# Kernel tuning notes

Measured on AMD Instinct MI355X. Metric: run time of the kernel, lower is better.

## Reference

```python
import jax, jax.numpy as jnp
import numpy as np

EPS = 1e-5

def _bn(x, g, b, m, v):
    # inference-mode BatchNorm2d over channel dim of NCHW
    inv = jax.lax.rsqrt(v + EPS)
    return (x - m[None, :, None, None]) * (g * inv)[None, :, None, None] + b[None, :, None, None]

def _conv1x1(x, w, b):
    # x: [B,C,H,W], w: [O,C], b: [O]
    return jnp.einsum('bchw,oc->bohw', x, w) + b[None, :, None, None]

def setup_inputs() -> dict:
    key = jax.random.key(0)
    ks = jax.random.split(key, 20)
    B, C, H, W = 16, 512, 64, 64
    C2, C4 = C // 2, C // 4
    d = {}
    d['x'] = jax.random.normal(ks[0], (B, C, H, W), jnp.float32)
    # query_conv_p1: Conv2d(512->256, k1) + BN + ReLU
    d['q1_w'] = jax.random.normal(ks[1], (C2, C), jnp.float32) * (1.0 / np.sqrt(C))
    d['q1_b'] = jax.random.normal(ks[2], (C2,), jnp.float32) * 0.01
    d['bn1_g'] = jax.random.uniform(ks[3], (C2,), jnp.float32, 0.5, 1.5)
    d['bn1_b'] = jax.random.normal(ks[4], (C2,), jnp.float32) * 0.01
    d['bn1_m'] = jax.random.normal(ks[5], (C2,), jnp.float32) * 0.01
    d['bn1_v'] = jax.random.uniform(ks[6], (C2,), jnp.float32, 0.5, 1.5)
    # query_conv_p2: Conv2d(256->128, k1) + BN + ReLU
    d['q2_w'] = jax.random.normal(ks[7], (C4, C2), jnp.float32) * (1.0 / np.sqrt(C2))
    d['q2_b'] = jax.random.normal(ks[8], (C4,), jnp.float32) * 0.01
    d['bn2_g'] = jax.random.uniform(ks[9], (C4,), jnp.float32, 0.5, 1.5)
    d['bn2_b'] = jax.random.normal(ks[10], (C4,), jnp.float32) * 0.01
    d['bn2_m'] = jax.random.normal(ks[11], (C4,), jnp.float32) * 0.01
    d['bn2_v'] = jax.random.uniform(ks[12], (C4,), jnp.float32, 0.5, 1.5)
    # py1_prop: Conv1d(256->256, k1)  (py2_prop is never used in forward)
    d['p1_w'] = jax.random.normal(ks[13], (C2, C2), jnp.float32) * (1.0 / np.sqrt(C2))
    d['p1_b'] = jax.random.normal(ks[14], (C2,), jnp.float32) * 0.01
    # fusion_conv: Conv2d(512->512, k3, pad 1) + BN + ReLU
    d['fus_w'] = jax.random.normal(ks[15], (C, C, 3, 3), jnp.float32) * (1.0 / np.sqrt(C * 9))
    d['fus_b'] = jax.random.normal(ks[16], (C,), jnp.float32) * 0.01
    d['bn3_g'] = jax.random.uniform(ks[17], (C,), jnp.float32, 0.5, 1.5)
    d['bn3_b'] = jax.random.normal(ks[18], (C,), jnp.float32) * 0.01
    d['bn3_m'] = jnp.zeros((C,), jnp.float32)
    d['bn3_v'] = jnp.ones((C,), jnp.float32)
    # gamma: torch init is zeros(1); use small random so the attention branch is live
    d['gamma'] = jax.random.normal(ks[19], (1,), jnp.float32) * 0.1
    return d

def reference(x, q1_w, q1_b, bn1_g, bn1_b, bn1_m, bn1_v,
              q2_w, q2_b, bn2_g, bn2_b, bn2_m, bn2_v,
              p1_w, p1_b, fus_w, fus_b, bn3_g, bn3_b, bn3_m, bn3_v, gamma):
    B, C, H, W = x.shape
    C2, C4 = C // 2, C // 4
    py1 = jax.nn.relu(_bn(_conv1x1(x, q1_w, q1_b), bn1_g, bn1_b, bn1_m, bn1_v))   # [B,256,H,W]
    py2 = jax.nn.relu(_bn(_conv1x1(py1, q2_w, q2_b), bn2_g, bn2_b, bn2_m, bn2_v))  # [B,128,H,W]
    pq1 = py1.reshape(B, C2, -1)   # [B,256,HW]
    pk1 = x.reshape(B, C, -1)      # [B,512,HW]
    # energy_py1 = pq1 @ pk1^T -> [B,256,512]; Conv1d(k1) over channel dim; permute -> [B,512,256]
    e1 = jnp.einsum('bcn,bdn->bcd', pq1, pk1)
    e1 = jnp.einsum('oc,bcd->bod', p1_w, e1) + p1_b[None, :, None]
    e1 = e1.transpose(0, 2, 1)     # [B,512,256]
    pq2 = py2.reshape(B, C4, -1)   # [B,128,HW]
    # energy_py2 = (pq2 @ py1^T).permute -> [B,256,128]; same py1_prop conv applied
    e2 = jnp.einsum('bcn,bdn->bcd', pq2, py1.reshape(B, C2, -1)).transpose(0, 2, 1)  # [B,256,128]
    e2 = jnp.einsum('oc,bcd->bod', p1_w, e2) + p1_b[None, :, None]                    # [B,256,128]
    energy = jnp.einsum('bce,bed->bcd', e1, e2)  # [B,512,128]
    energy_new = jnp.max(energy, axis=-1, keepdims=True) - energy
    attention = jax.nn.softmax(energy_new, axis=-1)  # [B,512,128]
    out = jnp.einsum('bcd,bdn->bcn', attention, pq2)  # [B,512,HW]
    out = out.reshape(B, C, H, W)
    out = gamma[0] * out + x
    out = jax.lax.conv_general_dilated(out, fus_w, window_strides=(1, 1),
                                       padding=((1, 1), (1, 1)),
                                       dimension_numbers=('NCHW', 'OIHW', 'NCHW'))
    out = out + fus_b[None, :, None, None]
    out = jax.nn.relu(_bn(out, bn3_g, bn3_b, bn3_m, bn3_v))
    return out
```

## Files before the change

### kernel.cpp

```cpp
#include <hip/hip_runtime.h>
#include <math.h>

#define BATCH 16
#define CH    512
#define CH2   256
#define CH4   128
#define HH    64
#define WW    64
#define HWSZ  4096
#define EPSV  1e-5f
#define HP 66
#define WP 66

typedef _Float16 f16x8 __attribute__((ext_vector_type(8)));
typedef float    f32x4 __attribute__((ext_vector_type(4)));

#define GLOBAL_AS __attribute__((address_space(1)))
#define LDS_AS    __attribute__((address_space(3)))

__device__ __forceinline__ void gload16(const void* g, void* l) {
    __builtin_amdgcn_global_load_lds((const GLOBAL_AS unsigned int*)g,
                                     (LDS_AS unsigned int*)l, 16, 0, 0);
}

__device__ __forceinline__ ushort f2h(float v) {
    _Float16 h = (_Float16)v;
    return *(ushort*)&h;
}
__device__ __forceinline__ float h2f(ushort u) {
    _Float16 h = *(_Float16*)&u;
    return (float)h;
}

__global__ void prep_params(
    const float* __restrict__ q1_b, const float* __restrict__ g1, const float* __restrict__ b1,
    const float* __restrict__ m1, const float* __restrict__ v1,
    const float* __restrict__ q2_b, const float* __restrict__ g2, const float* __restrict__ b2,
    const float* __restrict__ m2, const float* __restrict__ v2,
    const float* __restrict__ fus_b, const float* __restrict__ g3, const float* __restrict__ b3,
    const float* __restrict__ m3, const float* __restrict__ v3,
    float* __restrict__ s1, float* __restrict__ t1,
    float* __restrict__ s2, float* __restrict__ t2,
    float* __restrict__ s3, float* __restrict__ t3)
{
    int i = threadIdx.x;
    if (i < CH2) { float s = g1[i] * rsqrtf(v1[i] + EPSV); s1[i] = s; t1[i] = (q1_b[i] - m1[i]) * s + b1[i]; }
    if (i < CH4) { float s = g2[i] * rsqrtf(v2[i] + EPSV); s2[i] = s; t2[i] = (q2_b[i] - m2[i]) * s + b2[i]; }
    if (i < CH)  { float s = g3[i] * rsqrtf(v3[i] + EPSV); s3[i] = s; t3[i] = (fus_b[i] - m3[i]) * s + b3[i]; }
}

__global__ void transpose_p1(const float* __restrict__ p1w, float* __restrict__ p1T)
{
    int c = blockIdx.x;
    int o = threadIdx.x;
    p1T[c * CH2 + o] = p1w[o * CH2 + c];
}

__global__ void repack_w(const float* __restrict__ fw, ushort* __restrict__ wH)
{
    int o = blockIdx.x;
    int c = threadIdx.x;
    const float* src = fw + ((size_t)o * CH + c) * 9;
    #pragma unroll
    for (int t = 0; t < 9; ++t)
        wH[((size_t)t * CH + o) * CH + c] = f2h(src[t]);
}

__global__ void cvt_h(const float* __restrict__ s, ushort* __restrict__ d, int n)
{
    int i = blockIdx.x * blockDim.x + threadIdx.x;
    if (i < n) d[i] = f2h(s[i]);
}

__global__ void zero_buf(uint4* __restrict__ p, int n)
{
    const uint4 z = make_uint4(0u, 0u, 0u, 0u);
    for (int i = blockIdx.x * blockDim.x + threadIdx.x; i < n; i += gridDim.x * blockDim.x)
        p[i] = z;
}

__global__ __launch_bounds__(256)
void cvt_x(const float* __restrict__ x, ushort* __restrict__ xHc, ushort* __restrict__ xHp)
{
    __shared__ float t[64][68];
    const int b  = blockIdx.z;
    const int c0 = blockIdx.y * 64;
    const int p0 = blockIdx.x * 64;
    const int tid = threadIdx.x;
    const int tx = tid & 15, ty = tid >> 4;

    const float* xb = x + ((size_t)b * CH + c0) * HWSZ + p0;
    #pragma unroll
    for (int it = 0; it < 4; ++it) {
        const int r = ty + it * 16;
        float4 v = *(const float4*)&xb[(size_t)r * HWSZ + tx * 4];
        *(float4*)&t[r][tx * 4] = v;
        ushort4 u = make_ushort4(f2h(v.x), f2h(v.y), f2h(v.z), f2h(v.w));
        *(ushort4*)&xHc[((size_t)b * CH + c0 + r) * HWSZ + p0 + tx * 4] = u;
    }
    __syncthreads();
    #pragma unroll
    for (int it = 0; it < 4; ++it) {
        const int p = ty + it * 16;
        const int c = tx * 4;
        ushort4 u = make_ushort4(f2h(t[c + 0][p]), f2h(t[c + 1][p]),
                                 f2h(t[c + 2][p]), f2h(t[c + 3][p]));
        *(ushort4*)&xHp[((size_t)b * HWSZ + p0 + p) * CH + c0 + c] = u;
    }
}

template<int EPI>
__global__ __launch_bounds__(256)
void hgemm(const ushort* __restrict__ A, const ushort* __restrict__ B,
           void* __restrict__ C0, void* __restrict__ C1,
           int N, int KP, int ldA, int ldB, int ldHp,
           long sA, long sB, long sC0, long sC1, long pStride,
           const float* __restrict__ scale, const float* __restrict__ shift,
           const ushort* __restrict__ XHp, const float* __restrict__ gamma)
{
    __shared__ alignas(16) ushort As[4096];
    __shared__ alignas(16) ushort Bs[4096];

    const int b  = blockIdx.z & 15;
    const int pk = blockIdx.z >> 4;
    const int m0 = blockIdx.y * 128;
    const int n0 = blockIdx.x * 128;
    const int kBase = pk * KP;

    const int tid  = threadIdx.x;
    const int lane = tid & 63;
    const int wv   = tid >> 6;
    const int wm   = wv >> 1;
    const int wn   = wv & 1;

    const int cpart = (lane & 3) * 8;
    const int prow  = lane >> 2;
    const int rA0 = wv * 32 + prow;
    const int rA1 = rA0 + 16;

    const ushort* Ag = A + (size_t)b * sA;
    const ushort* Bg = B + (size_t)b * sB;
    const ushort* aSrc0 = Ag + (size_t)(m0 + rA0) * ldA + cpart + kBase;
    const ushort* aSrc1 = Ag + (size_t)(m0 + rA1) * ldA + cpart + kBase;
    const ushort* bSrc0 = Bg + (size_t)(n0 + rA0) * ldB + cpart + kBase;
    const ushort* bSrc1 = Bg + (size_t)(n0 + rA1) * ldB + cpart + kBase;
    ushort* AsW = &As[wv * 1024];
    ushort* BsW = &Bs[wv * 1024];

    const int fr = lane & 15, fg = lane >> 4;
    const int aOff = (wm * 64 + fr) * 32 + fg * 8;
    const int bOff = (wn * 64 + fr) * 32 + fg * 8;

    f32x4 acc[4][4];
    const f32x4 vzero = {0.f, 0.f, 0.f, 0.f};
    #pragma unroll
    for (int i = 0; i < 4; ++i)
        #pragma unroll
        for (int j = 0; j < 4; ++j) acc[i][j] = vzero;

    for (int k0 = 0; k0 < KP; k0 += 32) {
        gload16(aSrc0 + k0, AsW);
        gload16(aSrc1 + k0, AsW + 512);
        gload16(bSrc0 + k0, BsW);
        gload16(bSrc1 + k0, BsW + 512);
        __syncthreads();

        f16x8 aF[4], bF[4];
        #pragma unroll
        for (int mi = 0; mi < 4; ++mi) aF[mi] = *(const f16x8*)&As[aOff + mi * 512];
        #pragma unroll
        for (int ni = 0; ni < 4; ++ni) bF[ni] = *(const f16x8*)&Bs[bOff + ni * 512];
        #pragma unroll
        for (int mi = 0; mi < 4; ++mi)
            #pragma unroll
            for (int ni = 0; ni < 4; ++ni)
                acc[mi][ni] = __builtin_amdgcn_mfma_f32_16x16x32_f16(aF[mi], bF[ni], acc[mi][ni], 0, 0, 0);
        __syncthreads();
    }

    #pragma unroll
    for (int mi = 0; mi < 4; ++mi) {
        const int mBase = m0 + wm * 64 + mi * 16 + fg * 4;
        #pragma unroll
        for (int ni = 0; ni < 4; ++ni) {
            const int n = n0 + wn * 64 + ni * 16 + fr;
            if constexpr (EPI == 0) {
                ushort us[4];
                #pragma unroll
                for (int reg = 0; reg < 4; ++reg) {
                    const int m = mBase + reg;
                    float v = fmaxf(acc[mi][ni][reg] * scale[m] + shift[m], 0.0f);
                    us[reg] = f2h(v);
                    ((ushort*)C0)[(size_t)b * sC0 + (size_t)m * N + n] = us[reg];
                }
                *(ushort4*)&((ushort*)C1)[(size_t)b * sC1 + (size_t)n * ldHp + mBase] =
                    make_ushort4(us[0], us[1], us[2], us[3]);
            }
            if constexpr (EPI == 1) {
                float* C = (float*)C0 + pk * pStride + (size_t)b * sC0;
                #pragma unroll
                for (int reg = 0; reg < 4; ++reg)
                    C[(size_t)(mBase + reg) * N + n] = acc[mi][ni][reg];
            }
            if constexpr (EPI == 2) {
                const int h = n >> 6, w = n & 63;
                const float g = gamma[0];
                ushort4 xv = *(const ushort4*)&XHp[((size_t)b * HWSZ + n) * CH + mBase];
                ushort4 pk4;
                pk4.x = f2h(g * acc[mi][ni][0] + h2f(xv.x));
                pk4.y = f2h(g * acc[mi][ni][1] + h2f(xv.y));
                pk4.z = f2h(g * acc[mi][ni][2] + h2f(xv.z));
                pk4.w = f2h(g * acc[mi][ni][3] + h2f(xv.w));
                *(ushort4*)&((ushort*)C0)[((size_t)(b * HP + h + 1) * WP + (w + 1)) * CH + mBase] = pk4;
            }
        }
    }
}

__global__ void reduce_parts(float* __restrict__ dst, const float* __restrict__ src,
                             int n4, int parts, long pstride)
{
    for (int i = blockIdx.x * blockDim.x + threadIdx.x; i < n4; i += gridDim.x * blockDim.x) {
        float4 s = ((const float4*)src)[i];
        for (int p = 1; p < parts; ++p) {
            const float4 v = *(const float4*)&src[(size_t)p * pstride + (size_t)i * 4];
            s.x += v.x; s.y += v.y; s.z += v.z; s.w += v.w;
        }
        ((float4*)dst)[i] = s;
    }
}

template<int EPI>
__global__ __launch_bounds__(256)
void gemm_ab(const float* __restrict__ A, const float* __restrict__ Bm,
             float* __restrict__ Cm,
             int M, int N, int K,
             long sA, long sB, long sC,
             const float* __restrict__ shift)
{
    __shared__ float As[16][68];
    __shared__ float Bs[16][68];

    const int b   = blockIdx.z;
    const float* Ab = A  + (long)b * sA;
    const float* Bb = Bm + (long)b * sB;

    const int m0 = blockIdx.y * 64;
    const int n0 = blockIdx.x * 64;
    const int tid = threadIdx.x;
    const int tx = tid & 15;
    const int ty = tid >> 4;

    const int a_m = tid >> 2;
    const int a_k = (tid & 3) * 4;
    const int b_k = tid >> 4;
    const int b_n = (tid & 15) * 4;

    float acc[4][4] = {};

    for (int k0 = 0; k0 < K; k0 += 16) {
        float4 av = *(const float4*)&Ab[(long)(m0 + a_m) * K + k0 + a_k];
        float4 bv = *(const float4*)&Bb[(long)(k0 + b_k) * N + n0 + b_n];
        As[a_k + 0][a_m] = av.x;
        As[a_k + 1][a_m] = av.y;
        As[a_k + 2][a_m] = av.z;
        As[a_k + 3][a_m] = av.w;
        *(float4*)&Bs[b_k][b_n] = bv;
        __syncthreads();
        #pragma unroll
        for (int k = 0; k < 16; ++k) {
            float4 a4 = *(const float4*)&As[k][ty * 4];
            float4 b4 = *(const float4*)&Bs[k][tx * 4];
            float ar[4] = {a4.x, a4.y, a4.z, a4.w};
            float br[4] = {b4.x, b4.y, b4.z, b4.w};
            #pragma unroll
            for (int i = 0; i < 4; ++i)
                #pragma unroll
                for (int j = 0; j < 4; ++j)
                    acc[i][j] += ar[i] * br[j];
        }
        __syncthreads();
    }

    float* Cb = Cm + (long)b * sC;
    #pragma unroll
    for (int i = 0; i < 4; ++i) {
        const int m = m0 + ty * 4 + i;
        float v[4];
        #pragma unroll
        for (int j = 0; j < 4; ++j) {
            float val = acc[i][j];
            if constexpr (EPI == 2) { val = val + shift[n0 + tx * 4 + j]; }
            v[j] = val;
        }
        *(float4*)&Cb[(long)m * N + n0 + tx * 4] = make_float4(v[0], v[1], v[2], v[3]);
    }
}

__global__ __launch_bounds__(256)
void gemm_abT(const float* __restrict__ A, const float* __restrict__ Bm,
              float* __restrict__ Cm,
              int M, int N, int K,
              long sA, long sB, long sC,
              const float* __restrict__ shift)
{
    __shared__ float As[16][68];
    __shared__ float Bs[16][68];

    const int b   = blockIdx.z;
    const float* Ab = A  + (long)b * sA;
    const float* Bb = Bm + (long)b * sB;
    float*       Cb = Cm + (long)b * sC;

    const int m0 = blockIdx.y * 64;
    const int n0 = blockIdx.x * 64;
    const int tid = threadIdx.x;
    const int tx = tid & 15;
    const int ty = tid >> 4;

    const int r  = tid >> 2;
    const int kq = (tid & 3) * 4;

    float acc[4][4] = {};

    for (int k0 = 0; k0 < K; k0 += 16) {
        float4 av = *(const float4*)&Ab[(long)(m0 + r) * K + k0 + kq];
        float4 bv = *(const float4*)&Bb[(long)(n0 + r) * K + k0 + kq];
        As[kq + 0][r] = av.x; As[kq + 1][r] = av.y; As[kq + 2][r] = av.z; As[kq + 3][r] = av.w;
        Bs[kq + 0][r] = bv.x; Bs[kq + 1][r] = bv.y; Bs[kq + 2][r] = bv.z; Bs[kq + 3][r] = bv.w;
        __syncthreads();
        #pragma unroll
        for (int k = 0; k < 16; ++k) {
            float4 a4 = *(const float4*)&As[k][ty * 4];
            float4 b4 = *(const float4*)&Bs[k][tx * 4];
            float ar[4] = {a4.x, a4.y, a4.z, a4.w};
            float br[4] = {b4.x, b4.y, b4.z, b4.w};
            #pragma unroll
            for (int i = 0; i < 4; ++i)
                #pragma unroll
                for (int j = 0; j < 4; ++j)
                    acc[i][j] += ar[i] * br[j];
        }
        __syncthreads();
    }

    #pragma unroll
    for (int i = 0; i < 4; ++i) {
        const int m = m0 + ty * 4 + i;
        float v[4];
        #pragma unroll
        for (int j = 0; j < 4; ++j) v[j] = acc[i][j] + shift[m];
        *(float4*)&Cb[(long)m * N + n0 + tx * 4] = make_float4(v[0], v[1], v[2], v[3]);
    }
}

__global__ void softmax_rows(const float* __restrict__ e, ushort* __restrict__ attH)
{
    const int row  = blockIdx.x;
    const int lane = threadIdx.x;
    const float* p = e + (long)row * CH4;
    float a = p[lane];
    float c = p[lane + 64];
    float mn = fminf(a, c);
    #pragma unroll
    for (int off = 32; off; off >>= 1) mn = fminf(mn, __shfl_xor(mn, off));
    float ea = expf(mn - a);
    float ec = expf(mn - c);
    float s = ea + ec;
    #pragma unroll
    for (int off = 32; off; off >>= 1) s += __shfl_xor(s, off);
    float inv = 1.0f / s;
    attH[(long)row * CH4 + lane]      = f2h(ea * inv);
    attH[(long)row * CH4 + lane + 64] = f2h(ec * inv);
}

__global__ __launch_bounds__(256)
void conv3_mfma(const ushort* __restrict__ preH, const ushort* __restrict__ wH,
                const float* __restrict__ s3, const float* __restrict__ t3,
                float* __restrict__ outp)
{
    __shared__ alignas(16) ushort As[4096];
    __shared__ alignas(16) ushort Bs[4096];

    const int bid = blockIdx.x;
    const int lin = (bid & 7) * 256 + (bid >> 3);
    const int ob  = lin >> 9;
    const int pt  = lin & 511;
    const int b   = pt >> 5;
    const int h0  = (pt & 31) * 2;
    const int o0  = ob * 128;

    const int tid  = threadIdx.x;
    const int lane = tid & 63;
    const int wv   = tid >> 6;
    const int wm   = wv >> 1;
    const int wn   = wv & 1;

    const int cpart = (lane & 3) * 8;
    const int prow  = lane >> 2;
    const int pA0 = wv * 2, pA1 = pA0 + 1;
    const size_t aBase0 = (size_t)(o0 + pA0 * 16 + prow) * CH + cpart;
    const size_t aBase1 = (size_t)(o0 + pA1 * 16 + prow) * CH + cpart;
    const int P0 = pA0 * 16 + prow, P1 = pA1 * 16 + prow;
    const size_t bBase0 = ((size_t)(b * HP + h0 + (P0 >> 6)) * WP + (P0 & 63)) * CH + cpart;
    const size_t bBase1 = ((size_t)(b * HP + h0 + (P1 >> 6)) * WP + (P1 & 63)) * CH + cpart;
    ushort* AsW = &As[(size_t)wv * 1024];
    ushort* BsW = &Bs[(size_t)wv * 1024];

    const int fr = lane & 15, fg = lane >> 4;
    const int aOff = (wm * 64 + fr) * 32 + fg * 8;
    const int bOff = (wn * 64 + fr) * 32 + fg * 8;

    f32x4 acc[4][4];
    const f32x4 vzero = {0.f, 0.f, 0.f, 0.f};
    #pragma unroll
    for (int i = 0; i < 4; ++i)
        #pragma unroll
        for (int j = 0; j < 4; ++j) acc[i][j] = vzero;

    for (int t = 0; t < 9; ++t) {
        const int r = t / 3, s = t - r * 3;
        const size_t tOffA = (size_t)t * CH * CH;
        const size_t tOffB = (size_t)(r * WP + s) * CH;
        for (int c0 = 0; c0 < CH; c0 += 32) {
            gload16(wH   + tOffA + aBase0 + c0, AsW);
            gload16(wH   + tOffA + aBase1 + c0, AsW + 512);
            gload16(preH + tOffB + bBase0 + c0, BsW);
            gload16(preH + tOffB + bBase1 + c0, BsW + 512);
            __syncthreads();

            f16x8 aF[4], bF[4];
            #pragma unroll
            for (int mi = 0; mi < 4; ++mi) aF[mi] = *(const f16x8*)&As[aOff + mi * 512];
            #pragma unroll
            for (int ni = 0; ni < 4; ++ni) bF[ni] = *(const f16x8*)&Bs[bOff + ni * 512];
            #pragma unroll
            for (int mi = 0; mi < 4; ++mi)
                #pragma unroll
                for (int ni = 0; ni < 4; ++ni)
                    acc[mi][ni] = __builtin_amdgcn_mfma_f32_16x16x32_f16(aF[mi], bF[ni], acc[mi][ni], 0, 0, 0);
            __syncthreads();
        }
    }

    #pragma unroll
    for (int mi = 0; mi < 4; ++mi) {
        #pragma unroll
        for (int reg = 0; reg < 4; ++reg) {
            const int o = o0 + wm * 64 + mi * 16 + fg * 4 + reg;
            const float sc = s3[o], tt = t3[o];
            #pragma unroll
            for (int ni = 0; ni < 4; ++ni) {
                const int pix = wn * 64 + ni * 16 + fr;
                const float val = fmaxf(acc[mi][ni][reg] * sc + tt, 0.0f);
                outp[(size_t)(b * CH + o) * HWSZ + (h0 + (pix >> 6)) * WW + (pix & 63)] = val;
            }
        }
    }
}

extern "C" void kernel_launch(void* const* d_in, const int* in_sizes, int n_in,
                              void* d_out, int out_size, void* d_ws, size_t ws_size,
                              hipStream_t stream)
{
    const float* x     = (const float*)d_in[0];
    const float* q1_w  = (const float*)d_in[1];
    const float* q1_b  = (const float*)d_in[2];
    const float* bn1_g = (const float*)d_in[3];
    const float* bn1_b = (const float*)d_in[4];
    const float* bn1_m = (const float*)d_in[5];
    const float* bn1_v = (const float*)d_in[6];
    const float* q2_w  = (const float*)d_in[7];
    const float* q2_b  = (const float*)d_in[8];
    const float* bn2_g = (const float*)d_in[9];
    const float* bn2_b = (const float*)d_in[10];
    const float* bn2_m = (const float*)d_in[11];
    const float* bn2_v = (const float*)d_in[12];
    const float* p1_w  = (const float*)d_in[13];
    const float* p1_b  = (const float*)d_in[14];
    const float* fus_w = (const float*)d_in[15];
    const float* fus_b = (const float*)d_in[16];
    const float* bn3_g = (const float*)d_in[17];
    const float* bn3_b = (const float*)d_in[18];
    const float* bn3_m = (const float*)d_in[19];
    const float* bn3_v = (const float*)d_in[20];
    const float* gamma = (const float*)d_in[21];
    float* outp = (float*)d_out;

    float* ws = (float*)d_ws;
    size_t off = 0;
    ushort* py2Hp = (ushort*)(ws + off); off += (size_t)BATCH * HWSZ * CH4 / 2;
    ushort* attH  = (ushort*)(ws + off); off += (size_t)BATCH * CH * CH4 / 2;
    ushort* wH    = (ushort*)(ws + off); off += (size_t)9 * CH * CH / 2;
    ushort* q1_wH = (ushort*)(ws + off); off += (size_t)CH2 * CH / 2;
    ushort* q2_wH = (ushort*)(ws + off); off += (size_t)CH4 * CH2 / 2;
    float* e1T    = ws + off; off += (size_t)BATCH * CH * CH2;
    float* e2     = ws + off; off += (size_t)BATCH * CH4 * CH2;
    float* e2p    = ws + off; off += (size_t)BATCH * CH2 * CH4;
    float* p1T    = ws + off; off += (size_t)CH2 * CH2;
    float* e1Tparts = ws + off; off += 2 * (size_t)BATCH * CH * CH2;
    float* e1pt   = e1Tparts;
    float* energy = e1Tparts + (size_t)BATCH * CH * CH2;
    ushort* xHp   = (ushort*)(ws + off); off += (size_t)BATCH * HWSZ * CH / 2;
    float* R = ws + off; off += (size_t)5 * BATCH * HWSZ * CH2 / 2;
    ushort* py1Hc = (ushort*)R;
    ushort* py1Hp = py1Hc + (size_t)BATCH * HWSZ * CH2;
    ushort* py2Hc = py1Hp + (size_t)BATCH * HWSZ * CH2;
    ushort* preH  = (ushort*)R;
    float* xHcR = ws + off; off += (size_t)BATCH * HWSZ * CH / 2;
    ushort* xHc    = (ushort*)xHcR;
    float* e2parts = xHcR;
    float* s1 = ws + off; off += CH2;
    float* t1 = ws + off; off += CH2;
    float* s2 = ws + off; off += CH4;
    float* t2 = ws + off; off += CH4;
    float* s3 = ws + off; off += CH;
    float* t3 = ws + off; off += CH;

    const long sXc  = (long)CH  * HWSZ;
    const long sXp  = (long)HWSZ * CH;
    const long sP1c = (long)CH2 * HWSZ;
    const long sP1p = (long)HWSZ * CH2;
    const long sP2c = (long)CH4 * HWSZ;
    const long sP2p = (long)HWSZ * CH4;

    prep_params<<<1, 512, 0, stream>>>(q1_b, bn1_g, bn1_b, bn1_m, bn1_v,
                                       q2_b, bn2_g, bn2_b, bn2_m, bn2_v,
                                       fus_b, bn3_g, bn3_b, bn3_m, bn3_v,
                                       s1, t1, s2, t2, s3, t3);
    transpose_p1<<<CH2, CH2, 0, stream>>>(p1_w, p1T);
    repack_w<<<CH, CH, 0, stream>>>(fus_w, wH);
    cvt_h<<<(CH2 * CH + 255) / 256, 256, 0, stream>>>(q1_w, q1_wH, CH2 * CH);
    cvt_h<<<(CH4 * CH2 + 255) / 256, 256, 0, stream>>>(q2_w, q2_wH, CH4 * CH2);
    cvt_x<<<dim3(64, 8, BATCH), 256, 0, stream>>>(x, xHc, xHp);

    hgemm<0><<<dim3(32, 2, BATCH), 256, 0, stream>>>(
        q1_wH, xHp, py1Hc, py1Hp, HWSZ, CH, CH, CH, CH2,
        0, sXp, sP1c, sP1p, 0, s1, t1, nullptr, nullptr);

    hgemm<0><<<dim3(32, 1, BATCH), 256, 0, stream>>>(
        q2_wH, py1Hp, py2Hc, py2Hp, HWSZ, CH2, CH2, CH2, CH4,
        0, sP1p, sP2c, sP2p, 0, s2, t2, nullptr, nullptr);

    hgemm<1><<<dim3(2, 4, 2 * BATCH), 256, 0, stream>>>(
        xHc, py1Hc, e1Tparts, nullptr, CH2, 2048, HWSZ, HWSZ, 0,
        sXc, sP1c, (long)CH * CH2, 0, (long)BATCH * CH * CH2, nullptr, nullptr, nullptr, nullptr);
    reduce_parts<<<1024, 256, 0, stream>>>(e1T, e1Tparts,
        (int)((size_t)BATCH * CH * CH2 / 4), 2, (long)BATCH * CH * CH2);

    hgemm<1><<<dim3(2, 1, 8 * BATCH), 256, 0, stream>>>(
        py2Hc, py1Hc, e2parts, nullptr, CH2, 512, HWSZ, HWSZ, 0,
        sP2c, sP1c, (long)CH4 * CH2, 0, (long)BATCH * CH4 * CH2, nullptr, nullptr, nullptr, nullptr);
    reduce_parts<<<512, 256, 0, stream>>>(e2, e2parts,
        (int)((size_t)BATCH * CH4 * CH2 / 4), 8, (long)BATCH * CH4 * CH2);

    gemm_abT<<<dim3(2, 4, BATCH), 256, 0, stream>>>(
        p1_w, e2, e2p, CH2, CH4, CH2, 0, (long)CH4 * CH2, (long)CH2 * CH4, p1_b);

    gemm_ab<2><<<dim3(4, 8, BATCH), 256, 0, stream>>>(
        e1T, p1T, e1pt, CH, CH2, CH2, (long)CH * CH2, 0, (long)CH * CH2, p1_b);

    gemm_ab<3><<<dim3(2, 8, BATCH), 256, 0, stream>>>(
        e1pt, e2p, energy, CH, CH4, CH2, (long)CH * CH2, (long)CH2 * CH4, (long)CH * CH4,
        nullptr);

    softmax_rows<<<BATCH * CH, 64, 0, stream>>>(energy, attH);

    zero_buf<<<2048, 256, 0, stream>>>((uint4*)preH, (int)((size_t)BATCH * HP * WP * CH * 2 / 16));
    hgemm<2><<<dim3(32, 4, BATCH), 256, 0, stream>>>(
        attH, py2Hp, preH, nullptr, HWSZ, CH4, CH4, CH4, 0,
        (long)CH * CH4, sP2p, 0, 0, 0, nullptr, nullptr, xHp, gamma);

    conv3_mfma<<<2048, 256, 0, stream>>>(preH, wH, s3, t3, outp);
}
```

Measured before the change: 945.8 us.

## Reuse padded input row tile across all nine conv taps; zero only borders

```diff
diff --git a/kernel.cpp b/kernel.cpp
--- a/kernel.cpp
+++ b/kernel.cpp
@@ -72,11 +72,19 @@
     if (i < n) d[i] = f2h(s[i]);
 }
 
-__global__ void zero_buf(uint4* __restrict__ p, int n)
-{
+__global__ void zero_border(ushort* __restrict__ preH)
+{
+    int i = blockIdx.x * blockDim.x + threadIdx.x;
+    const int q  = i & 63;
+    const int px = (i >> 6) % 260;
+    const int b  = i / (260 * 64);
+    int hp, wp;
+    if (px < 66)       { hp = 0;            wp = px; }
+    else if (px < 132) { hp = 65;           wp = px - 66; }
+    else if (px < 196) { hp = px - 132 + 1; wp = 0; }
+    else               { hp = px - 196 + 1; wp = 65; }
     const uint4 z = make_uint4(0u, 0u, 0u, 0u);
-    for (int i = blockIdx.x * blockDim.x + threadIdx.x; i < n; i += gridDim.x * blockDim.x)
-        p[i] = z;
+    *(uint4*)&preH[((size_t)(b * HP + hp) * WP + wp) * CH + q * 8] = z;
 }
 
 __global__ __launch_bounds__(256)
@@ -375,12 +383,12 @@
 }
 
 __global__ __launch_bounds__(256)
-void conv3_mfma(const ushort* __restrict__ preH, const ushort* __restrict__ wH,
-                const float* __restrict__ s3, const float* __restrict__ t3,
-                float* __restrict__ outp)
-{
-    __shared__ alignas(16) ushort As[4096];
-    __shared__ alignas(16) ushort Bs[4096];
+void conv3_direct(const ushort* __restrict__ preH, const ushort* __restrict__ wH,
+                  const float* __restrict__ s3, const float* __restrict__ t3,
+                  float* __restrict__ outp)
+{
+    __shared__ alignas(16) ushort Pt[4 * 66 * 32];
+    __shared__ alignas(16) ushort Wl[128 * 32];
 
     const int bid = blockIdx.x;
     const int lin = (bid & 7) * 256 + (bid >> 3);
@@ -398,18 +406,17 @@
 
     const int cpart = (lane & 3) * 8;
     const int prow  = lane >> 2;
-    const int pA0 = wv * 2, pA1 = pA0 + 1;
-    const size_t aBase0 = (size_t)(o0 + pA0 * 16 + prow) * CH + cpart;
-    const size_t aBase1 = (size_t)(o0 + pA1 * 16 + prow) * CH + cpart;
-    const int P0 = pA0 * 16 + prow, P1 = pA1 * 16 + prow;
-    const size_t bBase0 = ((size_t)(b * HP + h0 + (P0 >> 6)) * WP + (P0 & 63)) * CH + cpart;
-    const size_t bBase1 = ((size_t)(b * HP + h0 + (P1 >> 6)) * WP + (P1 & 63)) * CH + cpart;
-    ushort* AsW = &As[(size_t)wv * 1024];
-    ushort* BsW = &Bs[(size_t)wv * 1024];
+
+    const size_t aBase0 = (size_t)(o0 + wv * 32 + prow) * CH + cpart;
+    const size_t aBase1 = aBase0 + (size_t)16 * CH;
+    ushort* WlW = &Wl[wv * 1024];
+
+    const size_t pRow0 = ((size_t)(b * HP + h0) * WP + 1) * CH;
+    const size_t pLane = (size_t)(wv * 16 + prow) * CH + cpart;
 
     const int fr = lane & 15, fg = lane >> 4;
     const int aOff = (wm * 64 + fr) * 32 + fg * 8;
-    const int bOff = (wn * 64 + fr) * 32 + fg * 8;
+    const int bLaneOff = (wn * 66 + fr) * 32 + fg * 8;
 
     f32x4 acc[4][4];
     const f32x4 vzero = {0.f, 0.f, 0.f, 0.f};
@@ -418,22 +425,32 @@
         #pragma unroll
         for (int j = 0; j < 4; ++j) acc[i][j] = vzero;
 
-    for (int t = 0; t < 9; ++t) {
-        const int r = t / 3, s = t - r * 3;
-        const size_t tOffA = (size_t)t * CH * CH;
-        const size_t tOffB = (size_t)(r * WP + s) * CH;
-        for (int c0 = 0; c0 < CH; c0 += 32) {
-            gload16(wH   + tOffA + aBase0 + c0, AsW);
-            gload16(wH   + tOffA + aBase1 + c0, AsW + 512);
-            gload16(preH + tOffB + bBase0 + c0, BsW);
-            gload16(preH + tOffB + bBase1 + c0, BsW + 512);
+    for (int c0 = 0; c0 < CH; c0 += 32) {
+        #pragma unroll
+        for (int rp = 0; rp < 4; ++rp)
+            gload16(preH + pRow0 + (size_t)rp * WP * CH + pLane + c0,
+                    &Pt[(rp * 66 + 1 + wv * 16) * 32]);
+        if (tid < 32) {
+            const int e  = tid >> 4;
+            const int rr = (tid >> 2) & 3;
+            const int q  = tid & 3;
+            const uint4 v = *(const uint4*)&preH[((size_t)(b * HP + h0 + rr) * WP + e * 65) * CH + c0 + q * 8];
+            *(uint4*)&Pt[(rr * 66 + e * 65) * 32 + q * 8] = v;
+        }
+
+        #pragma unroll
+        for (int t = 0; t < 9; ++t) {
+            const int r = t / 3, s = t - (t / 3) * 3;
+            gload16(wH + (size_t)t * CH * CH + aBase0 + c0, WlW);
+            gload16(wH + (size_t)t * CH * CH + aBase1 + c0, WlW + 512);
             __syncthreads();
 
             f16x8 aF[4], bF[4];
             #pragma unroll
-            for (int mi = 0; mi < 4; ++mi) aF[mi] = *(const f16x8*)&As[aOff + mi * 512];
-            #pragma unroll
-            for (int ni = 0; ni < 4; ++ni) bF[ni] = *(const f16x8*)&Bs[bOff + ni * 512];
+            for (int mi = 0; mi < 4; ++mi) aF[mi] = *(const f16x8*)&Wl[aOff + mi * 512];
+            #pragma unroll
+            for (int ni = 0; ni < 4; ++ni)
+                bF[ni] = *(const f16x8*)&Pt[bLaneOff + (r * 66 + s + ni * 16) * 32];
             #pragma unroll
             for (int mi = 0; mi < 4; ++mi)
                 #pragma unroll
@@ -566,10 +583,10 @@
 
     softmax_rows<<<BATCH * CH, 64, 0, stream>>>(energy, attH);
 
-    zero_buf<<<2048, 256, 0, stream>>>((uint4*)preH, (int)((size_t)BATCH * HP * WP * CH * 2 / 16));
+    zero_border<<<(BATCH * 260 * 64 + 255) / 256, 256, 0, stream>>>(preH);
     hgemm<2><<<dim3(32, 4, BATCH), 256, 0, stream>>>(
         attH, py2Hp, preH, nullptr, HWSZ, CH4, CH4, CH4, 0,
         (long)CH * CH4, sP2p, 0, 0, 0, nullptr, nullptr, xHp, gamma);
 
-    conv3_mfma<<<2048, 256, 0, stream>>>(preH, wH, s3, t3, outp);
-}
+    conv3_direct<<<2048, 256, 0, stream>>>(preH, wH, s3, t3, outp);
+}
```

After: 921.0 us. 2.6% less time.
